# Performance work log

Measured on AMD Instinct MI355X. Metric: run time of the kernel, lower is better.

Reference implementation:

```python
import jax, jax.numpy as jnp
import numpy as np


def _prelu(x, a):
    # torch.nn.PReLU with per-channel parameter a (broadcast over batch)
    return jnp.where(x >= 0, x, a * x)


def setup_inputs() -> dict:
    key = jax.random.key(0)
    ks = jax.random.split(key, 12)
    B = 8192
    dims = [512, 1024, 1024, 512]  # tardim
    E = 8                          # tctrl = modim[-1]
    scale = 0.02                   # keep activations well-scaled across 3 layers
    inp = {
        "x": jax.random.normal(ks[0], (B, dims[0]), dtype=jnp.float32),
        "weights": jax.random.uniform(ks[1], (E,), dtype=jnp.float32),
    }
    for i in range(3):
        din, dout = dims[i], dims[i + 1]
        inp[f"W{i}"] = jax.random.normal(ks[2 + 3 * i], (E, din, dout), dtype=jnp.float32) * scale
        inp[f"b{i}"] = jax.random.normal(ks[3 + 3 * i], (E, dout), dtype=jnp.float32) * scale
        inp[f"a{i}"] = jnp.full((dout,), 0.25, dtype=jnp.float32)  # PReLU init
    return inp


def reference(x, weights, W0, b0, a0, W1, b1, a1, W2, b2, a2):
    # mie.g: per layer, weighted sum over tctrl expert Linears, then PReLU.
    # sum_j (w_j/sum(w)) * (x @ W_j + b_j) == x @ (sum_j wn_j W_j) + sum_j wn_j b_j,
    # so pre-merge expert weights (tiny contraction) and do one GEMM per layer.
    wn = weights / jnp.sum(weights)  # [E]
    for W, b, a in ((W0, b0, a0), (W1, b1, a1), (W2, b2, a2)):
        Wm = jnp.einsum('e,eio->io', wn, W)  # merged weight [in, out]
        bm = jnp.einsum('e,eo->o', wn, b)    # merged bias   [out]
        x = _prelu(x @ Wm + bm, a)           # [B, out]
    return x
```

## Files before the change

### kernel.cpp

```cpp
#include <hip/hip_runtime.h>
#include <stdint.h>

typedef unsigned short u16;
typedef __attribute__((ext_vector_type(8))) short short8;
typedef __attribute__((ext_vector_type(4))) float float4v;

__device__ __forceinline__ u16 f2bf(float f) {
    union { float f; uint32_t u; } v; v.f = f;
    uint32_t r = v.u + 0x7fffu + ((v.u >> 16) & 1u);
    return (u16)(r >> 16);
}

__device__ __forceinline__ void gload16(const u16* g, u16* l) {
    __builtin_amdgcn_global_load_lds(
        (const __attribute__((address_space(1))) void*)g,
        (__attribute__((address_space(3))) void*)l, 16, 0, 0);
}

__global__ void cvt_f32_bf16(const float* __restrict__ x, u16* __restrict__ y) {
    int i = (blockIdx.x * 256 + threadIdx.x) * 4;
    float4 v = *(const float4*)(x + i);
    union { u16 s[4]; uint64_t q; } o;
    o.s[0] = f2bf(v.x); o.s[1] = f2bf(v.y); o.s[2] = f2bf(v.z); o.s[3] = f2bf(v.w);
    *(uint64_t*)(y + i) = o.q;
}

__global__ void merge_w(const float* __restrict__ W, const float* __restrict__ wts,
                        u16* __restrict__ Wt, int K, int N) {
    __shared__ float tile[32][33];
    float wn[8]; float s = 0.f;
    #pragma unroll
    for (int e = 0; e < 8; ++e) { wn[e] = wts[e]; s += wn[e]; }
    float inv = 1.0f / s;
    int o0 = blockIdx.x * 32, i0 = blockIdx.y * 32;
    int tx = threadIdx.x & 31, ty = threadIdx.x >> 5;
    #pragma unroll
    for (int s4 = 0; s4 < 4; ++s4) {
        int il = ty + s4 * 8;
        float acc = 0.f;
        #pragma unroll
        for (int e = 0; e < 8; ++e)
            acc += wn[e] * W[(size_t)e * K * N + (size_t)(i0 + il) * N + o0 + tx];
        tile[il][tx] = acc * inv;
    }
    __syncthreads();
    #pragma unroll
    for (int s4 = 0; s4 < 4; ++s4) {
        int ol = ty + s4 * 8;
        Wt[(size_t)(o0 + ol) * K + i0 + tx] = f2bf(tile[tx][ol]);
    }
}

__global__ void merge_bias(const float* __restrict__ wts,
                           const float* __restrict__ b0, const float* __restrict__ b1,
                           const float* __restrict__ b2, float* __restrict__ bm) {
    int t = blockIdx.x * 256 + threadIdx.x;
    if (t >= 2560) return;
    float wn[8]; float s = 0.f;
    #pragma unroll
    for (int e = 0; e < 8; ++e) { wn[e] = wts[e]; s += wn[e]; }
    float inv = 1.0f / s;
    const float* b; int o, stride;
    if (t < 1024)      { b = b0; o = t;        stride = 1024; }
    else if (t < 2048) { b = b1; o = t - 1024; stride = 1024; }
    else               { b = b2; o = t - 2048; stride = 512;  }
    float acc = 0.f;
    #pragma unroll
    for (int e = 0; e < 8; ++e) acc += wn[e] * b[e * stride + o];
    bm[t] = acc * inv;
}

template <bool OUT_F32>
__global__ __launch_bounds__(256) void gemm_bias_prelu(
    const u16* __restrict__ A, const u16* __restrict__ Bt,
    const float* __restrict__ bias, const float* __restrict__ alpha,
    void* __restrict__ outp, int M, int N, int K) {
    __shared__ __align__(16) u16 As[128 * 64];
    __shared__ __align__(16) u16 Bs[128 * 64];
    const int tid = threadIdx.x;
    const int bn = blockIdx.x, bm = blockIdx.y;

    const int r0 = tid >> 3;
    const int p  = tid & 7;
    const int c  = p ^ (r0 & 7);
    const u16* Ag = A  + (size_t)(bm * 128 + r0) * K + c * 8;
    const u16* Bg = Bt + (size_t)(bn * 128 + r0) * K + c * 8;
    u16* Al = As + tid * 8;
    u16* Bl = Bs + tid * 8;

    const int lane = tid & 63, w = tid >> 6;
    const int wm = (w >> 1) * 64, wn = (w & 1) * 64;
    const int l16 = lane & 15, quad = lane >> 4;
    const int xr = l16 & 7;
    const short8* As8 = (const short8*)As;
    const short8* Bs8 = (const short8*)Bs;

    float4v acc[4][4] = {};

    const int nk = K >> 6;
    for (int kt = 0; kt < nk; ++kt) {
        #pragma unroll
        for (int it = 0; it < 4; ++it) {
            gload16(Ag + (size_t)(it * 32) * K, Al + it * 2048);
            gload16(Bg + (size_t)(it * 32) * K, Bl + it * 2048);
        }
        __syncthreads();
        #pragma unroll
        for (int kk = 0; kk < 2; ++kk) {
            const int cb = kk * 4;
            short8 af[4], bf[4];
            #pragma unroll
            for (int mi = 0; mi < 4; ++mi)
                af[mi] = As8[(wm + mi * 16 + l16) * 8 + ((cb + quad) ^ xr)];
            #pragma unroll
            for (int ni = 0; ni < 4; ++ni)
                bf[ni] = Bs8[(wn + ni * 16 + l16) * 8 + ((cb + quad) ^ xr)];
            #pragma unroll
            for (int mi = 0; mi < 4; ++mi)
                #pragma unroll
                for (int ni = 0; ni < 4; ++ni)
                    acc[mi][ni] = __builtin_amdgcn_mfma_f32_16x16x32_bf16(
                        af[mi], bf[ni], acc[mi][ni], 0, 0, 0);
        }
        if (kt + 1 < nk) __syncthreads();
        Ag += 64; Bg += 64;
    }

    const int cbase = bn * 128 + wn + l16;
    float bv[4], av[4];
    #pragma unroll
    for (int ni = 0; ni < 4; ++ni) { bv[ni] = bias[cbase + ni * 16]; av[ni] = alpha[cbase + ni * 16]; }
    const int rbase = bm * 128 + wm + quad * 4;
    #pragma unroll
    for (int mi = 0; mi < 4; ++mi) {
        #pragma unroll
        for (int reg = 0; reg < 4; ++reg) {
            int r = rbase + mi * 16 + reg;
            #pragma unroll
            for (int ni = 0; ni < 4; ++ni) {
                float v = acc[mi][ni][reg] + bv[ni];
                v = v >= 0.f ? v : av[ni] * v;
                size_t idx = (size_t)r * N + cbase + ni * 16;
                if (OUT_F32) ((float*)outp)[idx] = v;
                else         ((u16*)outp)[idx] = f2bf(v);
            }
        }
    }
}

extern "C" void kernel_launch(void* const* d_in, const int* in_sizes, int n_in,
                              void* d_out, int out_size, void* d_ws, size_t ws_size,
                              hipStream_t stream) {
    const float* x   = (const float*)d_in[0];
    const float* wts = (const float*)d_in[1];
    const float* W0  = (const float*)d_in[2];
    const float* b0  = (const float*)d_in[3];
    const float* a0  = (const float*)d_in[4];
    const float* W1  = (const float*)d_in[5];
    const float* b1  = (const float*)d_in[6];
    const float* a1  = (const float*)d_in[7];
    const float* W2  = (const float*)d_in[8];
    const float* b2  = (const float*)d_in[9];
    const float* a2  = (const float*)d_in[10];
    float* out = (float*)d_out;

    char* ws = (char*)d_ws;
    u16*   xbf  = (u16*)ws;  ws += (size_t)8192 * 512 * 2;
    u16*   act1 = (u16*)ws;  ws += (size_t)8192 * 1024 * 2;
    u16*   act2 = (u16*)ws;  ws += (size_t)8192 * 1024 * 2;
    u16*   W0t  = (u16*)ws;  ws += (size_t)1024 * 512 * 2;
    u16*   W1t  = (u16*)ws;  ws += (size_t)1024 * 1024 * 2;
    u16*   W2t  = (u16*)ws;  ws += (size_t)512 * 1024 * 2;
    float* bm   = (float*)ws;

    cvt_f32_bf16<<<4096, 256, 0, stream>>>(x, xbf);
    merge_w<<<dim3(32, 16), 256, 0, stream>>>(W0, wts, W0t, 512, 1024);
    merge_w<<<dim3(32, 32), 256, 0, stream>>>(W1, wts, W1t, 1024, 1024);
    merge_w<<<dim3(16, 32), 256, 0, stream>>>(W2, wts, W2t, 1024, 512);
    merge_bias<<<10, 256, 0, stream>>>(wts, b0, b1, b2, bm);

    gemm_bias_prelu<false><<<dim3(8, 64), 256, 0, stream>>>(xbf,  W0t, bm,        a0, act1, 8192, 1024, 512);
    gemm_bias_prelu<false><<<dim3(8, 64), 256, 0, stream>>>(act1, W1t, bm + 1024, a1, act2, 8192, 1024, 1024);
    gemm_bias_prelu<true ><<<dim3(4, 64), 256, 0, stream>>>(act2, W2t, bm + 2048, a2, out,  8192, 512, 1024);
}
```

Baseline: 205.7 us.

## Fuse prep kernels into one launch and halve GEMM N-tile for more blocks

The input conversion, three weight merges and the bias merge are combined into a single kernel dispatched by block index, removing four launches. The GEMM tile shrinks from 128x128 to 128x64, doubling the grid (1024 blocks for the first two layers, 512 for the last), with launch_bounds set to target four blocks per CU. This aims to fill the 256 CUs better and raise occupancy to hide load latency. The cost is less data reuse per block, since each A tile is now loaded twice as often.

```diff
diff --git a/kernel.cpp b/kernel.cpp
--- a/kernel.cpp
+++ b/kernel.cpp
@@ -17,66 +17,75 @@
         (__attribute__((address_space(3))) void*)l, 16, 0, 0);
 }
 
-__global__ void cvt_f32_bf16(const float* __restrict__ x, u16* __restrict__ y) {
-    int i = (blockIdx.x * 256 + threadIdx.x) * 4;
-    float4 v = *(const float4*)(x + i);
-    union { u16 s[4]; uint64_t q; } o;
-    o.s[0] = f2bf(v.x); o.s[1] = f2bf(v.y); o.s[2] = f2bf(v.z); o.s[3] = f2bf(v.w);
-    *(uint64_t*)(y + i) = o.q;
-}
+__global__ __launch_bounds__(256) void prep_fused(
+    const float* __restrict__ x, u16* __restrict__ xbf,
+    const float* __restrict__ wts,
+    const float* __restrict__ W0, const float* __restrict__ W1, const float* __restrict__ W2,
+    u16* __restrict__ W0t, u16* __restrict__ W1t, u16* __restrict__ W2t,
+    const float* __restrict__ b0, const float* __restrict__ b1, const float* __restrict__ b2,
+    float* __restrict__ bm) {
+    __shared__ float tile[32][33];
+    const int b = blockIdx.x, tid = threadIdx.x;
 
-__global__ void merge_w(const float* __restrict__ W, const float* __restrict__ wts,
-                        u16* __restrict__ Wt, int K, int N) {
-    __shared__ float tile[32][33];
+    if (b < 4096) {
+        int i = (b * 256 + tid) * 4;
+        float4 v = *(const float4*)(x + i);
+        union { u16 s[4]; uint64_t q; } o;
+        o.s[0] = f2bf(v.x); o.s[1] = f2bf(v.y); o.s[2] = f2bf(v.z); o.s[3] = f2bf(v.w);
+        *(uint64_t*)(xbf + i) = o.q;
+        return;
+    }
+
     float wn[8]; float s = 0.f;
     #pragma unroll
     for (int e = 0; e < 8; ++e) { wn[e] = wts[e]; s += wn[e]; }
-    float inv = 1.0f / s;
-    int o0 = blockIdx.x * 32, i0 = blockIdx.y * 32;
-    int tx = threadIdx.x & 31, ty = threadIdx.x >> 5;
-    #pragma unroll
-    for (int s4 = 0; s4 < 4; ++s4) {
-        int il = ty + s4 * 8;
-        float acc = 0.f;
+    const float inv = 1.0f / s;
+
+    if (b < 6144) {
+        const float* W; u16* Wt; int K, N, lb;
+        if (b < 4608)      { W = W0; Wt = W0t; K = 512;  N = 1024; lb = b - 4096; }
+        else if (b < 5632) { W = W1; Wt = W1t; K = 1024; N = 1024; lb = b - 4608; }
+        else               { W = W2; Wt = W2t; K = 1024; N = 512;  lb = b - 5632; }
+        const int ntiles = N >> 5;
+        const int o0 = (lb % ntiles) * 32, i0 = (lb / ntiles) * 32;
+        const int tx = tid & 31, ty = tid >> 5;
         #pragma unroll
-        for (int e = 0; e < 8; ++e)
-            acc += wn[e] * W[(size_t)e * K * N + (size_t)(i0 + il) * N + o0 + tx];
-        tile[il][tx] = acc * inv;
+        for (int s4 = 0; s4 < 4; ++s4) {
+            int il = ty + s4 * 8;
+            float acc = 0.f;
+            #pragma unroll
+            for (int e = 0; e < 8; ++e)
+                acc += wn[e] * W[(size_t)e * K * N + (size_t)(i0 + il) * N + o0 + tx];
+            tile[il][tx] = acc * inv;
+        }
+        __syncthreads();
+        #pragma unroll
+        for (int s4 = 0; s4 < 4; ++s4) {
+            int ol = ty + s4 * 8;
+            Wt[(size_t)(o0 + ol) * K + i0 + tx] = f2bf(tile[tx][ol]);
+        }
+        return;
     }
-    __syncthreads();
-    #pragma unroll
-    for (int s4 = 0; s4 < 4; ++s4) {
-        int ol = ty + s4 * 8;
-        Wt[(size_t)(o0 + ol) * K + i0 + tx] = f2bf(tile[tx][ol]);
-    }
-}
 
-__global__ void merge_bias(const float* __restrict__ wts,
-                           const float* __restrict__ b0, const float* __restrict__ b1,
-                           const float* __restrict__ b2, float* __restrict__ bm) {
-    int t = blockIdx.x * 256 + threadIdx.x;
+    int t = (b - 6144) * 256 + tid;
     if (t >= 2560) return;
-    float wn[8]; float s = 0.f;
-    #pragma unroll
-    for (int e = 0; e < 8; ++e) { wn[e] = wts[e]; s += wn[e]; }
-    float inv = 1.0f / s;
-    const float* b; int o, stride;
-    if (t < 1024)      { b = b0; o = t;        stride = 1024; }
-    else if (t < 2048) { b = b1; o = t - 1024; stride = 1024; }
-    else               { b = b2; o = t - 2048; stride = 512;  }
+    const float* bp; int o, stride;
+    if (t < 1024)      { bp = b0; o = t;        stride = 1024; }
+    else if (t < 2048) { bp = b1; o = t - 1024; stride = 1024; }
+    else               { bp = b2; o = t - 2048; stride = 512;  }
     float acc = 0.f;
     #pragma unroll
-    for (int e = 0; e < 8; ++e) acc += wn[e] * b[e * stride + o];
+    for (int e = 0; e < 8; ++e) acc += wn[e] * bp[e * stride + o];
     bm[t] = acc * inv;
 }
 
 template <bool OUT_F32>
-__global__ __launch_bounds__(256) void gemm_bias_prelu(
+__global__ __launch_bounds__(256, 4) void gemm_bias_prelu(
     const u16* __restrict__ A, const u16* __restrict__ Bt,
     const float* __restrict__ bias, const float* __restrict__ alpha,
     void* __restrict__ outp, int M, int N, int K) {
     __shared__ __align__(16) u16 As[128 * 64];
-    __shared__ __align__(16) u16 Bs[128 * 64];
+    __shared__ __align__(16) u16 Bs[64 * 64];
     const int tid = threadIdx.x;
     const int bn = blockIdx.x, bm = blockIdx.y;
 
@@ -84,41 +93,42 @@
     const int p  = tid & 7;
     const int c  = p ^ (r0 & 7);
     const u16* Ag = A  + (size_t)(bm * 128 + r0) * K + c * 8;
-    const u16* Bg = Bt + (size_t)(bn * 128 + r0) * K + c * 8;
+    const u16* Bg = Bt + (size_t)(bn * 64  + r0) * K + c * 8;
     u16* Al = As + tid * 8;
     u16* Bl = Bs + tid * 8;
 
     const int lane = tid & 63, w = tid >> 6;
-    const int wm = (w >> 1) * 64, wn = (w & 1) * 64;
+    const int wm = (w >> 1) * 64, wncol = (w & 1) * 32;
     const int l16 = lane & 15, quad = lane >> 4;
     const int xr = l16 & 7;
     const short8* As8 = (const short8*)As;
     const short8* Bs8 = (const short8*)Bs;
 
-    float4v acc[4][4] = {};
+    float4v acc[4][2] = {};
 
     const int nk = K >> 6;
     for (int kt = 0; kt < nk; ++kt) {
         #pragma unroll
-        for (int it = 0; it < 4; ++it) {
+        for (int it = 0; it < 4; ++it)
             gload16(Ag + (size_t)(it * 32) * K, Al + it * 2048);
+        #pragma unroll
+        for (int it = 0; it < 2; ++it)
             gload16(Bg + (size_t)(it * 32) * K, Bl + it * 2048);
-        }
         __syncthreads();
         #pragma unroll
         for (int kk = 0; kk < 2; ++kk) {
             const int cb = kk * 4;
-            short8 af[4], bf[4];
+            short8 af[4], bf[2];
             #pragma unroll
             for (int mi = 0; mi < 4; ++mi)
                 af[mi] = As8[(wm + mi * 16 + l16) * 8 + ((cb + quad) ^ xr)];
             #pragma unroll
-            for (int ni = 0; ni < 4; ++ni)
-                bf[ni] = Bs8[(wn + ni * 16 + l16) * 8 + ((cb + quad) ^ xr)];
+            for (int ni = 0; ni < 2; ++ni)
+                bf[ni] = Bs8[(wncol + ni * 16 + l16) * 8 + ((cb + quad) ^ xr)];
             #pragma unroll
             for (int mi = 0; mi < 4; ++mi)
                 #pragma unroll
-                for (int ni = 0; ni < 4; ++ni)
+                for (int ni = 0; ni < 2; ++ni)
                     acc[mi][ni] = __builtin_amdgcn_mfma_f32_16x16x32_bf16(
                         af[mi], bf[ni], acc[mi][ni], 0, 0, 0);
         }
@@ -126,10 +136,10 @@
         Ag += 64; Bg += 64;
     }
 
-    const int cbase = bn * 128 + wn + l16;
-    float bv[4], av[4];
+    const int cbase = bn * 64 + wncol + l16;
+    float bv[2], av[2];
     #pragma unroll
-    for (int ni = 0; ni < 4; ++ni) { bv[ni] = bias[cbase + ni * 16]; av[ni] = alpha[cbase + ni * 16]; }
+    for (int ni = 0; ni < 2; ++ni) { bv[ni] = bias[cbase + ni * 16]; av[ni] = alpha[cbase + ni * 16]; }
     const int rbase = bm * 128 + wm + quad * 4;
     #pragma unroll
     for (int mi = 0; mi < 4; ++mi) {
@@ -137,7 +147,7 @@
         for (int reg = 0; reg < 4; ++reg) {
             int r = rbase + mi * 16 + reg;
             #pragma unroll
-            for (int ni = 0; ni < 4; ++ni) {
+            for (int ni = 0; ni < 2; ++ni) {
                 float v = acc[mi][ni][reg] + bv[ni];
                 v = v >= 0.f ? v : av[ni] * v;
                 size_t idx = (size_t)r * N + cbase + ni * 16;
@@ -173,13 +183,10 @@
     u16*   W2t  = (u16*)ws;  ws += (size_t)512 * 1024 * 2;
     float* bm   = (float*)ws;
 
-    cvt_f32_bf16<<<4096, 256, 0, stream>>>(x, xbf);
-    merge_w<<<dim3(32, 16), 256, 0, stream>>>(W0, wts, W0t, 512, 1024);
-    merge_w<<<dim3(32, 32), 256, 0, stream>>>(W1, wts, W1t, 1024, 1024);
-    merge_w<<<dim3(16, 32), 256, 0, stream>>>(W2, wts, W2t, 1024, 512);
-    merge_bias<<<10, 256, 0, stream>>>(wts, b0, b1, b2, bm);
+    prep_fused<<<6154, 256, 0, stream>>>(x, xbf, wts, W0, W1, W2, W0t, W1t, W2t,
+                                         b0, b1, b2, bm);
 
-    gemm_bias_prelu<false><<<dim3(8, 64), 256, 0, stream>>>(xbf,  W0t, bm,        a0, act1, 8192, 1024, 512);
-    gemm_bias_prelu<false><<<dim3(8, 64), 256, 0, stream>>>(act1, W1t, bm + 1024, a1, act2, 8192, 1024, 1024);
-    gemm_bias_prelu<true ><<<dim3(4, 64), 256, 0, stream>>>(act2, W2t, bm + 2048, a2, out,  8192, 512, 1024);
+    gemm_bias_prelu<false><<<dim3(16, 64), 256, 0, stream>>>(xbf,  W0t, bm,        a0, act1, 8192, 1024, 512);
+    gemm_bias_prelu<false><<<dim3(16, 64), 256, 0, stream>>>(act1, W1t, bm + 1024, a1, act2, 8192, 1024, 1024);
+    gemm_bias_prelu<true ><<<dim3(8, 64),  256, 0, stream>>>(act2, W2t, bm + 2048, a2, out,  8192, 512, 1024);
 }
```

Result: faster. 196.4 us (-4.5%).
